# Kernel optimization log

Hardware: AMD Instinct MI355X
Metric: run time of the kernel (lower is better)

The kernel has to match this reference:

```python
import jax, jax.numpy as jnp
import numpy as np

B, CTX, DRAFT, D = 2, 4096, 512, 2048
H, KVH, HD = 16, 4, 128
N_REP = H // KVH
EPS = 1e-6
THETA = 10000.0
SCALE = 1.0 / np.sqrt(HD).astype(np.float32)


def setup_inputs() -> dict:
    key = jax.random.key(0)
    ks = jax.random.split(key, 6)
    return {
        "draft_hidden": jax.random.normal(ks[0], (B, DRAFT, D), jnp.float32),
        "context_hidden": jax.random.normal(ks[1], (B, CTX, D), jnp.float32),
        "Wq": jax.random.normal(ks[2], (H * HD, D), jnp.float32) * 0.02,
        "Wk": jax.random.normal(ks[3], (KVH * HD, D), jnp.float32) * 0.02,
        "Wv": jax.random.normal(ks[4], (KVH * HD, D), jnp.float32) * 0.02,
        "Wo": jax.random.normal(ks[5], (D, H * HD), jnp.float32) * 0.02,
        "q_norm_w": jnp.ones((HD,), jnp.float32),
        "k_norm_w": jnp.ones((HD,), jnp.float32),
        "context_position_ids": jnp.broadcast_to(jnp.arange(CTX, dtype=jnp.int32), (B, CTX)),
        "draft_position_ids": jnp.broadcast_to(CTX + jnp.arange(DRAFT, dtype=jnp.int32), (B, DRAFT)),
    }


def _rms_norm(x, w):
    # per-head RMSNorm over last dim (head_dim), computed in fp32
    v = jnp.mean(jnp.square(x.astype(jnp.float32)), axis=-1, keepdims=True)
    return (w * (x.astype(jnp.float32) * jax.lax.rsqrt(v + EPS))).astype(x.dtype)


def _rotate_half(x):
    x1, x2 = jnp.split(x, 2, axis=-1)
    return jnp.concatenate((-x2, x1), axis=-1)


def _rope(x, pos):
    # x: [B, nH, S, HD], pos: [B, S] int -> cos/sin gathered per position
    inv_freq = 1.0 / (THETA ** (jnp.arange(0, HD, 2, dtype=jnp.float32) / HD))  # [HD/2]
    freqs = pos.astype(jnp.float32)[:, None, :, None] * inv_freq  # [B,1,S,HD/2]
    emb = jnp.concatenate((freqs, freqs), axis=-1)  # [B,1,S,HD]
    return x * jnp.cos(emb) + _rotate_half(x) * jnp.sin(emb)


def reference(draft_hidden, context_hidden, Wq, Wk, Wv, Wo, q_norm_w, k_norm_w,
              context_position_ids, draft_position_ids):
    bsz, draft_len, _ = draft_hidden.shape
    ctx_len = context_hidden.shape[1]
    total_len = ctx_len + draft_len

    # Q from draft hidden only
    q = (draft_hidden @ Wq.T).reshape(bsz, draft_len, H, HD)
    q = _rms_norm(q, q_norm_w).transpose(0, 2, 1, 3)  # [B,H,Sq,HD]

    # Dual-source KV: context then draft, shared projections
    kv_in = jnp.concatenate([context_hidden, draft_hidden], axis=1)  # [B,total,D]
    k = (kv_in @ Wk.T).reshape(bsz, total_len, KVH, HD)
    v = (kv_in @ Wv.T).reshape(bsz, total_len, KVH, HD).transpose(0, 2, 1, 3)
    k = _rms_norm(k, k_norm_w).transpose(0, 2, 1, 3)  # [B,KVH,total,HD]

    full_position_ids = jnp.concatenate([context_position_ids, draft_position_ids], axis=1)
    q = _rope(q, draft_position_ids)
    k = _rope(k, full_position_ids)

    # GQA expansion (repeat each kv head n_rep times contiguously)
    k = jnp.repeat(k, N_REP, axis=1)  # [B,H,total,HD]
    v = jnp.repeat(v, N_REP, axis=1)

    # full (unmasked) scaled dot-product attention, block_mask=None path
    scores = jnp.einsum('bhqd,bhkd->bhqk', q, k) * SCALE
    probs = jax.nn.softmax(scores, axis=-1)
    attn = jnp.einsum('bhqk,bhkd->bhqd', probs, v)  # [B,H,Sq,HD]

    attn = attn.transpose(0, 2, 1, 3).reshape(bsz, draft_len, H * HD)
    return attn @ Wo.T
```

## Files before the change

kernel.cpp:

```cpp
#include <hip/hip_runtime.h>
#include <stdint.h>

#define B_ 2
#define CTX_ 4096
#define DRAFT_ 512
#define D_ 2048
#define H_ 16
#define KVH_ 4
#define HD_ 128
#define TOT_ 4608
#define NSPLIT 4
#define SPLIT_LEN (TOT_ / NSPLIT)

using bf16x8 = __attribute__((ext_vector_type(8))) short;
using f32x4  = __attribute__((ext_vector_type(4))) float;
using f32x16 = __attribute__((ext_vector_type(16))) float;

__device__ __forceinline__ unsigned short f2bf(float x) {
  unsigned int u = __float_as_uint(x);
  u += 0x7fffu + ((u >> 16) & 1u);
  return (unsigned short)(u >> 16);
}

__device__ __forceinline__ unsigned cvtpk(float lo, float hi) {
  unsigned r;
  asm("v_cvt_pk_bf16_f32 %0, %1, %2" : "=v"(r) : "v"(lo), "v"(hi));
  return r;
}

__device__ __forceinline__ void gload16(const void* g, void* l) {
  __builtin_amdgcn_global_load_lds((const __attribute__((address_space(1))) void*)g,
                                   (__attribute__((address_space(3))) void*)l, 16, 0, 0);
}

__device__ __forceinline__ f32x16 vbroad16(float x) {
  f32x16 v;
#pragma unroll
  for (int i = 0; i < 16; ++i) v[i] = x;
  return v;
}

__global__ __launch_bounds__(256, 4)
void conv_kernel(const float* __restrict__ ctx, const float* __restrict__ draft,
                 const float* __restrict__ wq, const float* __restrict__ wk,
                 const float* __restrict__ wv, const float* __restrict__ wo,
                 unsigned short* __restrict__ kv, unsigned short* __restrict__ wqb,
                 unsigned short* __restrict__ wkb, unsigned short* __restrict__ wvb,
                 unsigned short* __restrict__ wob) {
  long t = (long)blockIdx.x * 256 + threadIdx.x;
  const long NKV = (long)B_ * TOT_ * D_ / 8;
  const long NWQ = 2048L * 2048 / 8;
  const long NWK = 512L * 2048 / 8;
  const float* src;
  unsigned short* dst;
  if (t < NKV) {
    long i = t * 8;
    int b = (int)(i / ((long)TOT_ * D_));
    long rem = i - (long)b * TOT_ * D_;
    int r = (int)(rem / D_);
    int c = (int)(rem - (long)r * D_);
    if (r < CTX_) src = ctx + ((long)(b * CTX_ + r)) * D_ + c;
    else          src = draft + ((long)(b * DRAFT_ + (r - CTX_))) * D_ + c;
    dst = kv + i;
  } else if (t < NKV + NWQ) {
    long l = t - NKV; src = wq + l * 8; dst = wqb + l * 8;
  } else if (t < NKV + NWQ + NWK) {
    long l = t - NKV - NWQ; src = wk + l * 8; dst = wkb + l * 8;
  } else if (t < NKV + NWQ + 2 * NWK) {
    long l = t - NKV - NWQ - NWK; src = wv + l * 8; dst = wvb + l * 8;
  } else {
    long l = t - NKV - NWQ - 2 * NWK; src = wo + l * 8; dst = wob + l * 8;
  }
  float4 a = ((const float4*)src)[0];
  float4 b4 = ((const float4*)src)[1];
  uint4 o;
  o.x = (unsigned)f2bf(a.x) | ((unsigned)f2bf(a.y) << 16);
  o.y = (unsigned)f2bf(a.z) | ((unsigned)f2bf(a.w) << 16);
  o.z = (unsigned)f2bf(b4.x) | ((unsigned)f2bf(b4.y) << 16);
  o.w = (unsigned)f2bf(b4.z) | ((unsigned)f2bf(b4.w) << 16);
  *((uint4*)dst) = o;
}

template <int BM, int BN>
__device__ __forceinline__ void gemm_body(const unsigned short* __restrict__ A,
                                          const unsigned short* __restrict__ W,
                                          float* __restrict__ C, int ld, int kLen,
                                          int N, unsigned short* lds) {
  constexpr int MT = BM / 32;
  constexpr int NT = BN / 32;
  constexpr int BUF = (BM + BN) * 64;
  const int tid = threadIdx.x;
  const int lane = tid & 63, wid = tid >> 6;
  const int g = lane >> 4, r16 = lane & 15;
  const int wm = wid >> 1, wn = wid & 1;

  f32x4 zero = {0.f, 0.f, 0.f, 0.f};
  f32x4 acc[MT][NT];
#pragma unroll
  for (int i = 0; i < MT; ++i)
#pragma unroll
    for (int j = 0; j < NT; ++j) acc[i][j] = zero;

  auto stage = [&](int kb, unsigned short* buf) {
    unsigned short* As = buf;
    unsigned short* Bs = buf + BM * 64;
#pragma unroll
    for (int is = 0; is < BM / 32; ++is) {
      int row = is * 32 + (tid >> 3);
      int sl = (tid & 7) ^ (row & 7);
      gload16(A + (long)row * ld + kb + sl * 8, As + is * 2048 + wid * 512);
    }
#pragma unroll
    for (int is = 0; is < BN / 32; ++is) {
      int row = is * 32 + (tid >> 3);
      int sl = (tid & 7) ^ (row & 7);
      gload16(W + (long)row * ld + kb + sl * 8, Bs + is * 2048 + wid * 512);
    }
  };

  stage(0, lds);
  const int nk = kLen >> 6;
  for (int t = 0; t < nk; ++t) {
    __syncthreads();
    if (t + 1 < nk) stage((t + 1) << 6, lds + ((t + 1) & 1) * BUF);
    unsigned short* As = lds + (t & 1) * BUF;
    unsigned short* Bs = As + BM * 64;
#pragma unroll
    for (int kh = 0; kh < 2; ++kh) {
      bf16x8 af[MT], bfr[NT];
#pragma unroll
      for (int i = 0; i < MT; ++i) {
        int row = wm * (BM / 2) + i * 16 + r16;
        int sl = (kh * 4 + g) ^ (row & 7);
        af[i] = *(const bf16x8*)(As + row * 64 + sl * 8);
      }
#pragma unroll
      for (int j = 0; j < NT; ++j) {
        int row = wn * (BN / 2) + j * 16 + r16;
        int sl = (kh * 4 + g) ^ (row & 7);
        bfr[j] = *(const bf16x8*)(Bs + row * 64 + sl * 8);
      }
#pragma unroll
      for (int i = 0; i < MT; ++i)
#pragma unroll
        for (int j = 0; j < NT; ++j)
          acc[i][j] = __builtin_amdgcn_mfma_f32_16x16x32_bf16(af[i], bfr[j], acc[i][j], 0, 0, 0);
    }
  }
#pragma unroll
  for (int i = 0; i < MT; ++i)
#pragma unroll
    for (int j = 0; j < NT; ++j)
#pragma unroll
      for (int e = 0; e < 4; ++e) {
        int row = wm * (BM / 2) + i * 16 + g * 4 + e;
        int col = wn * (BN / 2) + j * 16 + r16;
        C[(long)row * N + col] = acc[i][j][e];
      }
}

__global__ __launch_bounds__(256, 2)
void qkv_kernel(const unsigned short* __restrict__ kvb,
                const unsigned short* __restrict__ wqb,
                const unsigned short* __restrict__ wkvb, float* __restrict__ qraw,
                float* __restrict__ kvraw) {
  __shared__ unsigned short lds[2 * 256 * 64];
  int id = (blockIdx.x & 7) * 88 + (blockIdx.x >> 3);
  if (id < 128) {
    int b = id >> 6, mb = (id >> 4) & 3, nb = id & 15;
    const unsigned short* A = kvb + ((long)b * TOT_ + CTX_ + mb * 128) * 2048;
    const unsigned short* W = wqb + (long)nb * 128 * 2048;
    float* C = qraw + ((long)b * 512 + mb * 128) * 2048 + nb * 128;
    gemm_body<128, 128>(A, W, C, 2048, 2048, 2048, lds);
  } else {
    int id2 = id - 128;
    int mb = id2 >> 3, nb = id2 & 7;
    const unsigned short* A = kvb + (long)mb * 128 * 2048;
    const unsigned short* W = wkvb + (long)nb * 128 * 2048;
    float* C = kvraw + (long)mb * 128 * 1024 + nb * 128;
    gemm_body<128, 128>(A, W, C, 2048, 2048, 1024, lds);
  }
}

__global__ __launch_bounds__(256, 3)
void ogemm_kernel(const unsigned short* __restrict__ attb,
                  const unsigned short* __restrict__ wob, float* __restrict__ oP) {
  __shared__ unsigned short lds[2 * 192 * 64];
  int mb = blockIdx.x, nb = blockIdx.y, z = blockIdx.z;
  const unsigned short* A = attb + (long)mb * 64 * 2048 + z * 1024;
  const unsigned short* W = wob + (long)nb * 128 * 2048 + z * 1024;
  float* C = oP + (long)z * 1024 * 2048 + (long)mb * 64 * 2048 + nb * 128;
  gemm_body<64, 128>(A, W, C, 2048, 1024, 2048, lds);
}

__global__ __launch_bounds__(256, 4)
void addo_kernel(const float* __restrict__ oP, float* __restrict__ out) {
  long t = (long)blockIdx.x * 256 + threadIdx.x;
  float4 a = ((const float4*)oP)[t];
  float4 b = ((const float4*)(oP + 1024L * 2048))[t];
  ((float4*)out)[t] = make_float4(a.x + b.x, a.y + b.y, a.z + b.z, a.w + b.w);
}

__global__ __launch_bounds__(256, 4)
void post_kernel(const float* __restrict__ qraw, const float* __restrict__ kvraw,
                 const float* __restrict__ qw, const float* __restrict__ kw,
                 const int* __restrict__ cpos, const int* __restrict__ dpos,
                 unsigned short* __restrict__ qatt, unsigned short* __restrict__ katt,
                 unsigned short* __restrict__ vt) {
  const int QB = (B_ * DRAFT_ * H_) / 4;
  const int KB = (B_ * TOT_ * KVH_) / 4;
  int bid = blockIdx.x;
  int tid = threadIdx.x;
  int lane = tid & 63, wid = tid >> 6;
  if (bid < QB + KB) {
    bool isQ = (bid < QB);
    int row = (isQ ? bid : bid - QB) * 4 + wid;
    const float* src;
    const float* wnorm;
    int pos;
    float fold;
    unsigned short* dst;
    if (isQ) {
      int b = row >> 13;
      int r2 = row & 8191;
      int s = r2 >> 4, hh = r2 & 15;
      src = qraw + (long)row * 128;
      wnorm = qw;
      pos = dpos[b * DRAFT_ + s];
      fold = 0.08838834764831843f * 1.4426950408889634f;
      dst = qatt + ((long)(b * H_ + hh) * DRAFT_ + s) * 128;
    } else {
      int b = row / (TOT_ * KVH_);
      int r2 = row - b * (TOT_ * KVH_);
      int s = r2 >> 2, hh = r2 & 3;
      src = kvraw + ((long)(b * TOT_ + s)) * 1024 + hh * 128;
      wnorm = kw;
      pos = (s < CTX_) ? cpos[b * CTX_ + s] : dpos[b * DRAFT_ + (s - CTX_)];
      fold = 1.0f;
      dst = katt + ((long)(b * KVH_ + hh) * TOT_ + s) * 128;
    }
    float x1 = src[lane], x2 = src[lane + 64];
    float ss = x1 * x1 + x2 * x2;
#pragma unroll
    for (int off = 1; off < 64; off <<= 1) ss += __shfl_xor(ss, off);
    float rn = rsqrtf(ss * 0.0078125f + 1e-6f);
    float y1 = wnorm[lane] * x1 * rn;
    float y2 = wnorm[lane + 64] * x2 * rn;
    float invf = exp2f((float)lane * -0.20762050593046014f);
    float fr = (float)pos * invf;
    float sn, cs;
    sincosf(fr, &sn, &cs);
    dst[lane] = f2bf((y1 * cs - y2 * sn) * fold);
    dst[lane + 64] = f2bf((y2 * cs + y1 * sn) * fold);
  } else {
    long t = (long)(bid - (QB + KB)) * 256 + tid;
    int d = (int)(t & 127);
    int rest = (int)(t >> 7);
    int sc = rest % 576, bk = rest / 576;
    int b = bk >> 2, kvh = bk & 3;
    int s0 = sc * 8;
    const float* src = kvraw + ((long)(b * TOT_ + s0)) * 1024 + 512 + kvh * 128 + d;
    unsigned int o[4];
#pragma unroll
    for (int jj = 0; jj < 4; ++jj) {
      unsigned short lo = f2bf(src[(2 * jj) * 1024]);
      unsigned short hi = f2bf(src[(2 * jj + 1) * 1024]);
      o[jj] = (unsigned)lo | ((unsigned)hi << 16);
    }
    int k0 = s0 & 63;
    long dstbase = ((long)(bk * 128 + d)) * TOT_ + (s0 & ~63) + (k0 & 48) + ((k0 & 8) >> 1);
    *(uint2*)(vt + dstbase) = make_uint2(o[0], o[1]);
    *(uint2*)(vt + dstbase + 8) = make_uint2(o[2], o[3]);
  }
}

__global__ __launch_bounds__(256, 2)
void attn_kernel(const unsigned short* __restrict__ Q, const unsigned short* __restrict__ Kt,
                 const unsigned short* __restrict__ Vt, float* __restrict__ pO,
                 float* __restrict__ pL) {
  __shared__ unsigned short lds[2 * 16384];
  const int tid = threadIdx.x, lane = tid & 63, wid = tid >> 6;
  const int hi = lane >> 5, l31 = lane & 31;
  int sw = ((blockIdx.x & 7) << 6) | (blockIdx.x >> 3);
  const int q0 = sw & 3, h = (sw >> 2) & 15, z = sw >> 6;
  const int b = z >> 2, split = z & 3;
  const int kvh = h >> 2;
  const float M = 16.4f;

  const unsigned short* Qb =
      Q + ((long)(b * H_ + h) * DRAFT_ + q0 * 128 + wid * 32) * 128;
  bf16x8 qf[8];
#pragma unroll
  for (int ks = 0; ks < 8; ++ks)
    qf[ks] = *(const bf16x8*)(Qb + l31 * 128 + ks * 16 + hi * 8);

  f32x16 acc[4];
#pragma unroll
  for (int nb = 0; nb < 4; ++nb) acc[nb] = vbroad16(0.f);
  float l_run = 0.0f;

  const unsigned short* Kbase = Kt + (long)(b * KVH_ + kvh) * TOT_ * 128;
  const unsigned short* Vbase = Vt + (long)(b * KVH_ + kvh) * 128L * TOT_;

  auto stage = [&](int s0, int c) {
    unsigned short* Ks = lds + c * 16384;
    unsigned short* Vs = Ks + 8192;
#pragma unroll
    for (int is = 0; is < 4; ++is) {
      int row = is * 16 + (tid >> 4);
      int sl = (tid & 15) ^ (row & 7);
      gload16(Kbase + (long)(s0 + row) * 128 + sl * 8, Ks + is * 2048 + wid * 512);
    }
#pragma unroll
    for (int is = 0; is < 4; ++is) {
      int d = is * 32 + (tid >> 3);
      int sl = (tid & 7) ^ (d & 7);
      gload16(Vbase + (long)d * TOT_ + s0 + sl * 8, Vs + is * 2048 + wid * 512);
    }
  };

  const int sBeg = split * SPLIT_LEN;
  const int NTile = SPLIT_LEN / 64;
  stage(sBeg, 0);
  int cur = 0;
  for (int t = 0; t < NTile; ++t) {
    if (t + 1 < NTile) {
      stage(sBeg + (t + 1) * 64, cur ^ 1);
      asm volatile("s_waitcnt vmcnt(8)" ::: "memory");
    } else {
      asm volatile("s_waitcnt vmcnt(0)" ::: "memory");
    }
    __builtin_amdgcn_s_barrier();
    __builtin_amdgcn_sched_barrier(0);
    const char* KsB = (const char*)(lds + cur * 16384);
    const char* VsB = KsB + 16384;

    f32x16 st0 = vbroad16(-M), st1 = vbroad16(-M);
    __builtin_amdgcn_s_setprio(1);
#pragma unroll
    for (int ks = 0; ks < 8; ++ks) {
      int gsl = ks * 2 + hi;
      bf16x8 a0 = *(const bf16x8*)(KsB + l31 * 256 + ((gsl ^ (l31 & 7)) * 16));
      bf16x8 a1 = *(const bf16x8*)(KsB + (32 + l31) * 256 + ((gsl ^ (l31 & 7)) * 16));
      st0 = __builtin_amdgcn_mfma_f32_32x32x16_bf16(a0, qf[ks], st0, 0, 0, 0);
      st1 = __builtin_amdgcn_mfma_f32_32x32x16_bf16(a1, qf[ks], st1, 0, 0, 0);
    }
    __builtin_amdgcn_s_setprio(0);

    float l_own = 0.0f;
    unsigned pkA[8], pkB[8];
#pragma unroll
    for (int m = 0; m < 8; ++m) {
      float e0 = exp2f(st0[2 * m]), e1 = exp2f(st0[2 * m + 1]);
      l_own += e0 + e1;
      pkA[m] = cvtpk(e0, e1);
    }
#pragma unroll
    for (int m = 0; m < 8; ++m) {
      float e0 = exp2f(st1[2 * m]), e1 = exp2f(st1[2 * m + 1]);
      l_own += e0 + e1;
      pkB[m] = cvtpk(e0, e1);
    }
    l_run += l_own;

    union { unsigned u[4]; bf16x8 v; } pf[4];
#pragma unroll
    for (int m = 0; m < 4; ++m) {
      pf[0].u[m] = pkA[m];
      pf[1].u[m] = pkA[m + 4];
      pf[2].u[m] = pkB[m];
      pf[3].u[m] = pkB[m + 4];
    }
    __builtin_amdgcn_s_setprio(1);
#pragma unroll
    for (int nb = 0; nb < 4; ++nb) {
      int d = nb * 32 + l31;
#pragma unroll
      for (int ks2 = 0; ks2 < 4; ++ks2) {
        bf16x8 a = *(const bf16x8*)(VsB + d * 128 + (((ks2 * 2 + hi) ^ (d & 7)) * 16));
        acc[nb] = __builtin_amdgcn_mfma_f32_32x32x16_bf16(a, pf[ks2].v, acc[nb], 0, 0, 0);
      }
    }
    __builtin_amdgcn_s_setprio(0);
    __builtin_amdgcn_sched_barrier(0);
    __builtin_amdgcn_s_barrier();
    cur ^= 1;
  }
  l_run += __shfl_xor(l_run, 32);

  const long R = (long)B_ * H_ * DRAFT_;
  const int q = q0 * 128 + wid * 32 + l31;
  const long rowIdx = ((long)(b * H_ + h)) * DRAFT_ + q;
  const long pbase = ((long)split * R + rowIdx) * 128;
#pragma unroll
  for (int nb = 0; nb < 4; ++nb)
#pragma unroll
    for (int r4 = 0; r4 < 4; ++r4) {
      int d0 = nb * 32 + 8 * r4 + 4 * hi;
      float4 v = make_float4(acc[nb][4 * r4 + 0], acc[nb][4 * r4 + 1],
                             acc[nb][4 * r4 + 2], acc[nb][4 * r4 + 3]);
      *(float4*)(pO + pbase + d0) = v;
    }
  if (hi == 0) pL[(long)split * R + rowIdx] = l_run;
}

__global__ __launch_bounds__(256, 4)
void acomb_kernel(const float* __restrict__ pO, const float* __restrict__ pL,
                  unsigned short* __restrict__ attb) {
  const long R = (long)B_ * H_ * DRAFT_;
  int row = blockIdx.x * 2 + (threadIdx.x >> 7);
  int d = threadIdx.x & 127;
  float ltot = 0.0f, o = 0.0f;
#pragma unroll
  for (int i = 0; i < NSPLIT; ++i) {
    ltot += pL[(long)i * R + row];
    o += pO[((long)i * R + row) * 128 + d];
  }
  o /= ltot;
  int bh = row >> 9, q = row & 511;
  int b = bh >> 4, h = bh & 15;
  attb[(((long)(b * 512 + q) * 16 + h)) * 128 + d] = f2bf(o);
}

extern "C" void kernel_launch(void* const* d_in, const int* in_sizes, int n_in,
                              void* d_out, int out_size, void* d_ws, size_t ws_size,
                              hipStream_t stream) {
  const float* draft = (const float*)d_in[0];
  const float* ctx = (const float*)d_in[1];
  const float* Wq = (const float*)d_in[2];
  const float* Wk = (const float*)d_in[3];
  const float* Wv = (const float*)d_in[4];
  const float* Wo = (const float*)d_in[5];
  const float* qw = (const float*)d_in[6];
  const float* kw = (const float*)d_in[7];
  const int* cpos = (const int*)d_in[8];
  const int* dpos = (const int*)d_in[9];

  char* ws = (char*)d_ws;
  unsigned short* kvb = (unsigned short*)(ws + 0);
  float* oP = (float*)(ws + 0);
  unsigned short* wqb = (unsigned short*)(ws + 37748736);
  unsigned short* wkb = (unsigned short*)(ws + 46137344);
  unsigned short* wvb = (unsigned short*)(ws + 48234496);
  unsigned short* wob = (unsigned short*)(ws + 50331648);
  float* qraw = (float*)(ws + 58720256);
  float* kvraw = (float*)(ws + 67108864);
  float* pO = (float*)(ws + 67108864);
  float* pL = (float*)(ws + 100663296);
  unsigned short* qatt = (unsigned short*)(ws + 104857600);
  unsigned short* katt = (unsigned short*)(ws + 109051904);
  unsigned short* vtb = (unsigned short*)(ws + 118489088);
  unsigned short* attb = (unsigned short*)(ws + 127926272);

  conv_kernel<<<dim3(14336), 256, 0, stream>>>(ctx, draft, Wq, Wk, Wv, Wo, kvb, wqb,
                                               wkb, wvb, wob);
  qkv_kernel<<<dim3(704), 256, 0, stream>>>(kvb, wqb, wkb, qraw, kvraw);
  post_kernel<<<dim3(15616), 256, 0, stream>>>(qraw, kvraw, qw, kw, cpos, dpos, qatt,
                                               katt, vtb);
  attn_kernel<<<dim3(512), 256, 0, stream>>>(qatt, katt, vtb, pO, pL);
  acomb_kernel<<<dim3(8192), 256, 0, stream>>>(pO, pL, attb);
  ogemm_kernel<<<dim3(16, 16, 2), 256, 0, stream>>>(attb, wob, oP);
  addo_kernel<<<dim3(2048), 256, 0, stream>>>(oP, (float*)d_out);
}
```

Measured before the change: 180.9 us.

## Double attention KV splits and drop LDS double buffering for higher occupancy

Raises the number of KV splits in the split-K attention from 4 to 8, so the grid grows to 1024 blocks on the 256-CU MI355X. LDS is cut to a single buffer, each tile is now loaded synchronously, and launch bounds allow 3 blocks per CU. Partial outputs go to two workspace regions, and the combine kernel sums all eight. In exchange, each tile load is no longer overlapped with compute, and the combine step reads twice as many partial outputs.

New measurement: 298.8 us. 1.65x slower.

```diff
diff --git a/kernel.cpp b/kernel.cpp
--- a/kernel.cpp
+++ b/kernel.cpp
@@ -9,7 +9,7 @@
 #define KVH_ 4
 #define HD_ 128
 #define TOT_ 4608
-#define NSPLIT 4
+#define NSPLIT 8
 #define SPLIT_LEN (TOT_ / NSPLIT)
 
 using bf16x8 = __attribute__((ext_vector_type(8))) short;
@@ -274,16 +274,18 @@
   }
 }
 
-__global__ __launch_bounds__(256, 2)
+__global__ __launch_bounds__(256, 3)
 void attn_kernel(const unsigned short* __restrict__ Q, const unsigned short* __restrict__ Kt,
-                 const unsigned short* __restrict__ Vt, float* __restrict__ pO,
-                 float* __restrict__ pL) {
-  __shared__ unsigned short lds[2 * 16384];
+                 const unsigned short* __restrict__ Vt, float* __restrict__ pOa,
+                 float* __restrict__ pOb, float* __restrict__ pL) {
+  __shared__ unsigned short lds[16384];
+  unsigned short* Ks = lds;
+  unsigned short* Vs = lds + 8192;
   const int tid = threadIdx.x, lane = tid & 63, wid = tid >> 6;
   const int hi = lane >> 5, l31 = lane & 31;
-  int sw = ((blockIdx.x & 7) << 6) | (blockIdx.x >> 3);
+  int sw = ((blockIdx.x & 7) << 7) | (blockIdx.x >> 3);
   const int q0 = sw & 3, h = (sw >> 2) & 15, z = sw >> 6;
-  const int b = z >> 2, split = z & 3;
+  const int b = z >> 3, split = z & 7;
   const int kvh = h >> 2;
   const float M = 16.4f;
 
@@ -302,9 +304,7 @@
   const unsigned short* Kbase = Kt + (long)(b * KVH_ + kvh) * TOT_ * 128;
   const unsigned short* Vbase = Vt + (long)(b * KVH_ + kvh) * 128L * TOT_;
 
-  auto stage = [&](int s0, int c) {
-    unsigned short* Ks = lds + c * 16384;
-    unsigned short* Vs = Ks + 8192;
+  auto stage = [&](int s0) {
 #pragma unroll
     for (int is = 0; is < 4; ++is) {
       int row = is * 16 + (tid >> 4);
@@ -321,19 +321,13 @@
 
   const int sBeg = split * SPLIT_LEN;
   const int NTile = SPLIT_LEN / 64;
-  stage(sBeg, 0);
-  int cur = 0;
   for (int t = 0; t < NTile; ++t) {
-    if (t + 1 < NTile) {
-      stage(sBeg + (t + 1) * 64, cur ^ 1);
-      asm volatile("s_waitcnt vmcnt(8)" ::: "memory");
-    } else {
-      asm volatile("s_waitcnt vmcnt(0)" ::: "memory");
-    }
+    stage(sBeg + t * 64);
+    asm volatile("s_waitcnt vmcnt(0)" ::: "memory");
     __builtin_amdgcn_s_barrier();
     __builtin_amdgcn_sched_barrier(0);
-    const char* KsB = (const char*)(lds + cur * 16384);
-    const char* VsB = KsB + 16384;
+    const char* KsB = (const char*)Ks;
+    const char* VsB = (const char*)Vs;
 
     f32x16 st0 = vbroad16(-M), st1 = vbroad16(-M);
     __builtin_amdgcn_s_setprio(1);
@@ -384,14 +378,14 @@
     __builtin_amdgcn_s_setprio(0);
     __builtin_amdgcn_sched_barrier(0);
     __builtin_amdgcn_s_barrier();
-    cur ^= 1;
   }
   l_run += __shfl_xor(l_run, 32);
 
   const long R = (long)B_ * H_ * DRAFT_;
   const int q = q0 * 128 + wid * 32 + l31;
   const long rowIdx = ((long)(b * H_ + h)) * DRAFT_ + q;
-  const long pbase = ((long)split * R + rowIdx) * 128;
+  float* pO = (split < 4) ? pOa : pOb;
+  const long pbase = ((long)(split & 3) * R + rowIdx) * 128;
 #pragma unroll
   for (int nb = 0; nb < 4; ++nb)
 #pragma unroll
@@ -405,16 +399,21 @@
 }
 
 __global__ __launch_bounds__(256, 4)
-void acomb_kernel(const float* __restrict__ pO, const float* __restrict__ pL,
-                  unsigned short* __restrict__ attb) {
+void acomb_kernel(const float* __restrict__ pOa, const float* __restrict__ pOb,
+                  const float* __restrict__ pL, unsigned short* __restrict__ attb) {
   const long R = (long)B_ * H_ * DRAFT_;
   int row = blockIdx.x * 2 + (threadIdx.x >> 7);
   int d = threadIdx.x & 127;
   float ltot = 0.0f, o = 0.0f;
 #pragma unroll
-  for (int i = 0; i < NSPLIT; ++i) {
+  for (int i = 0; i < 4; ++i) {
     ltot += pL[(long)i * R + row];
-    o += pO[((long)i * R + row) * 128 + d];
+    o += pOa[((long)i * R + row) * 128 + d];
+  }
+#pragma unroll
+  for (int i = 0; i < 4; ++i) {
+    ltot += pL[(long)(i + 4) * R + row];
+    o += pOb[((long)i * R + row) * 128 + d];
   }
   o /= ltot;
   int bh = row >> 9, q = row & 511;
@@ -438,6 +437,7 @@
 
   char* ws = (char*)d_ws;
   unsigned short* kvb = (unsigned short*)(ws + 0);
+  float* pOa = (float*)(ws + 0);
   float* oP = (float*)(ws + 0);
   unsigned short* wqb = (unsigned short*)(ws + 37748736);
   unsigned short* wkb = (unsigned short*)(ws + 46137344);
@@ -445,7 +445,7 @@
   unsigned short* wob = (unsigned short*)(ws + 50331648);
   float* qraw = (float*)(ws + 58720256);
   float* kvraw = (float*)(ws + 67108864);
-  float* pO = (float*)(ws + 67108864);
+  float* pOb = (float*)(ws + 67108864);
   float* pL = (float*)(ws + 100663296);
   unsigned short* qatt = (unsigned short*)(ws + 104857600);
   unsigned short* katt = (unsigned short*)(ws + 109051904);
@@ -457,8 +457,8 @@
   qkv_kernel<<<dim3(704), 256, 0, stream>>>(kvb, wqb, wkb, qraw, kvraw);
   post_kernel<<<dim3(15616), 256, 0, stream>>>(qraw, kvraw, qw, kw, cpos, dpos, qatt,
                                                katt, vtb);
-  attn_kernel<<<dim3(512), 256, 0, stream>>>(qatt, katt, vtb, pO, pL);
-  acomb_kernel<<<dim3(8192), 256, 0, stream>>>(pO, pL, attb);
+  attn_kernel<<<dim3(1024), 256, 0, stream>>>(qatt, katt, vtb, pOa, pOb, pL);
+  acomb_kernel<<<dim3(8192), 256, 0, stream>>>(pOa, pOb, pL, attb);
   ogemm_kernel<<<dim3(16, 16, 2), 256, 0, stream>>>(attb, wob, oP);
   addo_kernel<<<dim3(2048), 256, 0, stream>>>(oP, (float*)d_out);
 }
```
